# Kernel tuning notes

Measured on AMD Instinct MI355X. Metric: run time of the kernel, lower is better.

## Reference

```python
import jax, jax.numpy as jnp
import numpy as np

N = 40000   # nodes
E = 150000  # edges (before self-loops)
G = 128     # graphs in batch
V = 20000   # vocab
D = 512     # embedding/hidden dim
H = 4       # heads (layers 0,1)
C = 128     # per-head channels (H*C = D)


def setup_inputs() -> dict:
    key = jax.random.key(0)
    ks = jax.random.split(key, 64)
    n = lambda i, shp, s=0.05: jax.random.normal(ks[i], shp, dtype=jnp.float32) * s
    inp = {}
    inp['node_ids'] = jax.random.randint(ks[0], (N,), 0, V, dtype=jnp.int32)
    inp['edge_index'] = jax.random.randint(ks[1], (2, E), 0, N, dtype=jnp.int32)
    inp['batch'] = jnp.sort(jax.random.randint(ks[2], (N,), 0, G, dtype=jnp.int32))
    inp['emb'] = n(3, (V, D), 0.02)
    # GAT layer 0: D -> H x C, concat
    inp['W0'] = n(4, (D, H * C)); inp['as0'] = n(5, (H, C)); inp['ad0'] = n(6, (H, C)); inp['b0'] = n(7, (D,), 0.01)
    # GAT layer 1: D -> H x C, concat
    inp['W1'] = n(8, (D, H * C)); inp['as1'] = n(9, (H, C)); inp['ad1'] = n(10, (H, C)); inp['b1'] = n(11, (D,), 0.01)
    inp['W2'] = n(12, (D, D)); inp['as2'] = n(13, (1, D)); inp['ad2'] = n(14, (1, D)); inp['b2'] = n(15, (D,), 0.01)
    # danger head
    inp['dW1'] = n(16, (D, D)); inp['db1'] = n(17, (D,), 0.01)
    inp['dg1'] = 1.0 + n(18, (D,), 0.02); inp['dbt1'] = n(19, (D,), 0.02)
    inp['drm1'] = n(20, (D,), 0.02); inp['drv1'] = jax.random.uniform(ks[21], (D,)) + 0.5
    inp['dW2'] = n(22, (D, D // 2)); inp['db2'] = n(23, (D // 2,), 0.01)
    inp['dg2'] = 1.0 + n(24, (D // 2,), 0.02); inp['dbt2'] = n(25, (D // 2,), 0.02)
    inp['drm2'] = n(26, (D // 2,), 0.02); inp['drv2'] = jax.random.uniform(ks[27], (D // 2,)) + 0.5
    inp['dW3'] = n(28, (D // 2, 1)); inp['db3'] = n(29, (1,), 0.01)
    # synergy head
    inp['sW1'] = n(30, (D, D)); inp['sb1'] = n(31, (D,), 0.01)
    inp['sg1'] = 1.0 + n(32, (D,), 0.02); inp['sbt1'] = n(33, (D,), 0.02)
    inp['srm1'] = n(34, (D,), 0.02); inp['srv1'] = jax.random.uniform(ks[35], (D,)) + 0.5
    inp['sW2'] = n(36, (D, D // 2)); inp['sb2'] = n(37, (D // 2,), 0.01)
    inp['sg2'] = 1.0 + n(38, (D // 2,), 0.02); inp['sbt2'] = n(39, (D // 2,), 0.02)
    inp['srm2'] = n(40, (D // 2,), 0.02); inp['srv2'] = jax.random.uniform(ks[41], (D // 2,)) + 0.5
    inp['sW3'] = n(42, (D // 2, 1)); inp['sb3'] = n(43, (1,), 0.01)
    return inp


def _gat(x, W, a_src, a_dst, bias, src, dst, heads, ch, concat):
    # PyG GATConv (eval): linear, per-head additive attention, softmax over
    # incoming edges per destination node, scatter-add aggregate.
    n_nodes = x.shape[0]
    h = (x @ W).reshape(n_nodes, heads, ch)              # [N,H,C]
    e_s = jnp.sum(h * a_src, axis=-1)                    # [N,H]
    e_d = jnp.sum(h * a_dst, axis=-1)                    # [N,H]
    e = jax.nn.leaky_relu(e_s[src] + e_d[dst], 0.2)      # [E,H]
    m = jax.ops.segment_max(e, dst, num_segments=n_nodes)
    m = jnp.where(jnp.isfinite(m), m, 0.0)
    p = jnp.exp(e - m[dst])
    s = jax.ops.segment_sum(p, dst, num_segments=n_nodes)
    alpha = p / (s[dst] + 1e-16)                         # [E,H]
    out = jax.ops.segment_sum(h[src] * alpha[:, :, None], dst, num_segments=n_nodes)
    out = out.reshape(n_nodes, heads * ch) if concat else out.mean(axis=1)
    return out + bias


def _bn(x, g, b, rm, rv):
    return (x - rm) * jax.lax.rsqrt(rv + 1e-5) * g + b


def _head(p, W1, b1, g1, bt1, rm1, rv1, W2, b2, g2, bt2, rm2, rv2, W3, b3):
    z = jax.nn.relu(_bn(p @ W1 + b1, g1, bt1, rm1, rv1))
    z = jax.nn.relu(_bn(z @ W2 + b2, g2, bt2, rm2, rv2))
    return jax.nn.sigmoid(z @ W3 + b3)


def reference(node_ids, edge_index, batch, emb, W0, as0, ad0, b0, W1, as1, ad1, b1, W2, as2, ad2, b2, dW1, db1, dg1, dbt1, drm1, drv1, dW2, db2, dg2, dbt2, drm2, drv2, dW3, db3, sW1, sb1, sg1, sbt1, srm1, srv1, sW2, sb2, sg2, sbt2, srm2, srv2, sW3, sb3):
    loops = jnp.arange(N, dtype=edge_index.dtype)
    src = jnp.concatenate([edge_index[0], loops])
    dst = jnp.concatenate([edge_index[1], loops])
    x = emb[node_ids]                                    # [N,D]
    # layer 0 (no residual)
    x = jax.nn.relu(_gat(x, W0, as0, ad0, b0, src, dst, H, C, True))
    # layer 1 (+residual)
    x = x + jax.nn.relu(_gat(x, W1, as1, ad1, b1, src, dst, H, C, True))
    # layer 2 (+residual)
    x = x + jax.nn.relu(_gat(x, W2, as2, ad2, b2, src, dst, 1, D, False))
    # global mean pool per graph
    sums = jax.ops.segment_sum(x, batch, num_segments=G)
    cnt = jax.ops.segment_sum(jnp.ones((N,), x.dtype), batch, num_segments=G)
    pooled = sums / jnp.maximum(cnt, 1.0)[:, None]       # [G,D]
    danger = _head(pooled, dW1, db1, dg1, dbt1, drm1, drv1, dW2, db2, dg2, dbt2, drm2, drv2, dW3, db3)
    synergy = _head(pooled, sW1, sb1, sg1, sbt1, srm1, srv1, sW2, sb2, sg2, sbt2, srm2, srv2, sW3, sb3)
    return danger, synergy
```

## Files before the change

### kernel.cpp

```cpp
#include <hip/hip_runtime.h>
#include <hip/hip_bf16.h>
#include <stdint.h>

#define NN 40000
#define EE 150000
#define ET 190000
#define GG 128
#define DD 512
#define MP 40064
#define PS 16
#define GNB 1252
#define GNBF 1248
#define WB 192
#define CW 32

typedef __hip_bfloat16 bf16;
typedef __attribute__((ext_vector_type(8))) short s16x8;
typedef __attribute__((ext_vector_type(4))) float f32v4;

__device__ __forceinline__ float b2f(bf16 v) { return __bfloat162float(v); }
__device__ __forceinline__ bf16  f2b(float v) { return __float2bfloat16(v); }
__device__ __forceinline__ unsigned f2bu(float v) {
    bf16 b = __float2bfloat16(v);
    return (unsigned)*(unsigned short*)&b;
}
__device__ __forceinline__ float lo16(unsigned u) { return __uint_as_float(u << 16); }
__device__ __forceinline__ float hi16(unsigned u) { return __uint_as_float(u & 0xffff0000u); }
__device__ __forceinline__ float s2f(short s) {
    return __uint_as_float(((unsigned)(unsigned short)s) << 16);
}

__device__ __forceinline__ void gl_lds16(const void* g, void* l) {
    __builtin_amdgcn_global_load_lds(
        (const __attribute__((address_space(1))) unsigned int*)g,
        (__attribute__((address_space(3))) unsigned int*)l, 16, 0, 0);
}

__global__ __launch_bounds__(256) void k_prep(const float* __restrict__ W0,
                                              const float* __restrict__ W1,
                                              const float* __restrict__ W2,
                                              bf16* __restrict__ Wt0,
                                              bf16* __restrict__ Wt1,
                                              bf16* __restrict__ Wt2,
                                              const int* __restrict__ ids,
                                              const float4* __restrict__ emb4,
                                              bf16* __restrict__ xb) {
    __shared__ float tile[64][65];
    int b = blockIdx.x, tid = threadIdx.x;
    if (b < WB) {
        int wi = b >> 6, tl = b & 63;
        const float* W; bf16* Wt;
        if (wi == 0)      { W = W0; Wt = Wt0; }
        else if (wi == 1) { W = W1; Wt = Wt1; }
        else              { W = W2; Wt = Wt2; }
        int n0 = (tl & 7) * 64, k0 = (tl >> 3) * 64;
        int rr = tid >> 4, cc = (tid & 15) * 4;
        #pragma unroll
        for (int i = 0; i < 4; i++) {
            int k = k0 + i * 16 + rr;
            float4 v = *(const float4*)(W + (size_t)k * DD + n0 + cc);
            tile[cc + 0][i * 16 + rr] = v.x;
            tile[cc + 1][i * 16 + rr] = v.y;
            tile[cc + 2][i * 16 + rr] = v.z;
            tile[cc + 3][i * 16 + rr] = v.w;
        }
        __syncthreads();
        #pragma unroll
        for (int i = 0; i < 4; i++) {
            int nl = i * 16 + rr;
            ushort4 o;
            o.x = (unsigned short)f2bu(tile[nl][cc + 0]);
            o.y = (unsigned short)f2bu(tile[nl][cc + 1]);
            o.z = (unsigned short)f2bu(tile[nl][cc + 2]);
            o.w = (unsigned short)f2bu(tile[nl][cc + 3]);
            *(ushort4*)(Wt + (size_t)(n0 + nl) * DD + k0 + cc) = o;
        }
    } else {
        int t = (b - WB) * 256 + tid;
        int n = t >> 7, c = t & 127;
        if (n >= NN) return;
        int id = ids[n];
        float4 v = emb4[(size_t)id * 128 + c];
        ushort4 u;
        u.x = (unsigned short)f2bu(v.x); u.y = (unsigned short)f2bu(v.y);
        u.z = (unsigned short)f2bu(v.z); u.w = (unsigned short)f2bu(v.w);
        *(ushort4*)(xb + (size_t)n * DD + c * 4) = u;
    }
}

__global__ __launch_bounds__(256) void k_fill_fixed(const int* __restrict__ esrc,
                                                    const int* __restrict__ edst,
                                                    int* __restrict__ deg,
                                                    int* __restrict__ csrf) {
    int e = blockIdx.x * 256 + threadIdx.x;
    if (e >= ET) return;
    int dst, src;
    if (e < EE) { dst = edst[e]; src = esrc[e]; }
    else        { dst = e - EE;  src = dst; }
    int slot = atomicAdd(&deg[dst], 1);
    if (slot < CW) csrf[dst * CW + slot] = src;
}

template <int H>
__global__ __launch_bounds__(256) void k_gemm_mfma(const bf16* __restrict__ A,
                                                   const bf16* __restrict__ Bt,
                                                   bf16* __restrict__ C,
                                                   const float* __restrict__ a_s,
                                                   const float* __restrict__ a_d,
                                                   float* __restrict__ es,
                                                   float* __restrict__ ed) {
    constexpr int K = DD, N = DD;
    __shared__ bf16 smem[4 * 128 * 64];
    bf16* lA0 = smem;
    bf16* lB0 = smem + 8192;
    bf16* lA1 = smem + 16384;
    bf16* lB1 = smem + 24576;
    int tid = threadIdx.x, lane = tid & 63, quad = lane >> 4, l16 = lane & 15;
    int w = tid >> 6;

    int bid = blockIdx.x, mt, nt;
    if (bid >= GNBF) { mt = MP / 128 - 1; nt = bid - GNBF; }
    else { nt = (bid & 31) >> 3; mt = (bid >> 5) * 8 + (bid & 7); }
    int m0 = mt * 128, n0 = nt * 128;
    int wm = (w & 1) * 64, wn = (w >> 1) * 64;

    int l8 = lane >> 3, c16 = (lane & 7) << 4;
    int scol = c16 ^ (l8 << 4);
    const char* pAg = (const char*)A + (size_t)(m0 + w * 32 + l8) * (K * 2) + scol;
    const char* pBg = (const char*)Bt + (size_t)(n0 + w * 32 + l8) * (K * 2) + scol;
    char* dA0 = (char*)lA0 + w * 4096;
    char* dB0 = (char*)lB0 + w * 4096;
    char* dA1 = (char*)lA1 + w * 4096;
    char* dB1 = (char*)lB1 + w * 4096;

    int aoff[2][4], boff[2][4];
    #pragma unroll
    for (int kk = 0; kk < 2; kk++)
        #pragma unroll
        for (int i = 0; i < 4; i++) {
            int qb = (kk * 4 + quad) << 4;
            int rowA = wm + i * 16 + l16;
            int rowB = wn + i * 16 + l16;
            aoff[kk][i] = rowA * 64 + ((qb ^ ((rowA & 7) << 4)) >> 1);
            boff[kk][i] = rowB * 64 + ((qb ^ ((rowB & 7) << 4)) >> 1);
        }

    f32v4 zero = 0;
    f32v4 acc[4][4];
    #pragma unroll
    for (int i = 0; i < 4; i++)
        #pragma unroll
        for (int j = 0; j < 4; j++) acc[i][j] = zero;

    auto stage = [&](int kb, char* dA, char* dB) {
        #pragma unroll
        for (int i = 0; i < 4; i++) {
            gl_lds16(pAg + i * 8192 + kb, dA + i * 1024);
            gl_lds16(pBg + i * 8192 + kb, dB + i * 1024);
        }
    };
    auto compute = [&](const bf16* bA, const bf16* bB) {
        #pragma unroll
        for (int kk = 0; kk < 2; kk++) {
            s16x8 a[4], b[4];
            #pragma unroll
            for (int i = 0; i < 4; i++) a[i] = *(const s16x8*)(bA + aoff[kk][i]);
            #pragma unroll
            for (int j = 0; j < 4; j++) b[j] = *(const s16x8*)(bB + boff[kk][j]);
            #pragma unroll
            for (int i = 0; i < 4; i++)
                #pragma unroll
                for (int j = 0; j < 4; j++)
                    acc[i][j] = __builtin_amdgcn_mfma_f32_16x16x32_bf16(a[i], b[j], acc[i][j], 0, 0, 0);
        }
    };

    stage(0, dA0, dB0);
    __syncthreads();
    #pragma unroll
    for (int k0 = 0; k0 < K; k0 += 128) {
        stage((k0 + 64) * 2, dA1, dB1);
        compute(lA0, lB0);
        __syncthreads();
        if (k0 + 128 < K) stage((k0 + 128) * 2, dA0, dB0);
        compute(lA1, lB1);
        __syncthreads();
    }

    float* asl = (float*)(smem + 8192);
    float* adl = asl + 128;
    if (tid < 128) asl[tid] = a_s[n0 + tid];
    else           adl[tid - 128] = a_d[n0 + tid - 128];

    constexpr int ESTR = 136;
    bf16* ebuf = smem;
    int lrB = (w & 1) * 16 + quad * 4;
    int lr = tid >> 3, cc8 = (tid & 7) * 16;
    int grow = m0 + (lr >> 4) * 64 + (lr & 15);
    #pragma unroll
    for (int i = 0; i < 4; i++) {
        __syncthreads();
        #pragma unroll
        for (int j = 0; j < 4; j++) {
            int col = wn + j * 16 + l16;
            #pragma unroll
            for (int r = 0; r < 4; r++)
                ebuf[(lrB + r) * ESTR + col] = f2b(acc[i][j][r]);
        }
        __syncthreads();
        s16x8 v0 = *(s16x8*)(ebuf + lr * ESTR + cc8);
        s16x8 v1 = *(s16x8*)(ebuf + lr * ESTR + cc8 + 8);
        float ses = 0.f, sed = 0.f;
        #pragma unroll
        for (int k = 0; k < 8; k++) {
            float x = s2f(v0[k]);
            ses += x * asl[cc8 + k];
            sed += x * adl[cc8 + k];
        }
        #pragma unroll
        for (int k = 0; k < 8; k++) {
            float x = s2f(v1[k]);
            ses += x * asl[cc8 + 8 + k];
            sed += x * adl[cc8 + 8 + k];
        }
        #pragma unroll
        for (int off = 1; off < 8; off <<= 1) {
            ses += __shfl_xor(ses, off, 64);
            sed += __shfl_xor(sed, off, 64);
        }
        int row = grow + i * 16;
        if ((tid & 7) == 0) {
            if (H == 4) {
                es[(size_t)row * 4 + nt] = ses;
                ed[(size_t)row * 4 + nt] = sed;
            } else {
                es[(size_t)nt * MP + row] = ses;
                ed[(size_t)nt * MP + row] = sed;
            }
        }
        size_t o = (size_t)row * N + n0 + cc8;
        *(s16x8*)(C + o) = v0;
        *(s16x8*)(C + o + 8) = v1;
    }
}

template <int H, bool RES>
__global__ __launch_bounds__(256) void k_gat_aggregate(const bf16* __restrict__ h,
                                                       const float* __restrict__ es,
                                                       const float* __restrict__ ed,
                                                       const int* __restrict__ degv,
                                                       const int* __restrict__ csrf,
                                                       const float* __restrict__ bias,
                                                       bf16* __restrict__ xb) {
    __shared__ int   s_src[8][32];
    __shared__ float s_a[8][32 * H];
    __shared__ int   s_deg[8];
    int tid = threadIdx.x, w = tid >> 6, lane = tid & 63;
    int half = lane >> 5, el = lane & 31;
    int nb = blockIdx.x * 8;
    {
        int ln = w * 2 + half;
        int node = nb + ln;
        int deg = degv[node];
        if (deg > CW) deg = CW;
        if (el == 0) s_deg[ln] = deg;
        float edl[H];
        if (H == 4) {
            #pragma unroll
            for (int hh = 0; hh < H; hh++) edl[hh] = ed[node * H + hh];
        } else {
            edl[0] = ed[node] + ed[MP + node] + ed[2 * MP + node] + ed[3 * MP + node];
        }
        float e_h[H];
        #pragma unroll
        for (int hh = 0; hh < H; hh++) e_h[hh] = -1e30f;
        if (el < deg) {
            int src = csrf[node * CW + el];
            s_src[ln][el] = src;
            if (H == 4) {
                float4 e4 = *(const float4*)(es + (size_t)src * 4);
                float t4[4] = {e4.x, e4.y, e4.z, e4.w};
                #pragma unroll
                for (int hh = 0; hh < 4; hh++) {
                    float e = t4[hh] + edl[hh];
                    e_h[hh] = e > 0.f ? e : 0.2f * e;
                }
            } else {
                float esv = es[src] + es[MP + src] + es[2 * MP + src] + es[3 * MP + src];
                float e = esv + edl[0];
                e_h[0] = e > 0.f ? e : 0.2f * e;
            }
        }
        float m[H];
        #pragma unroll
        for (int hh = 0; hh < H; hh++) m[hh] = e_h[hh];
        #pragma unroll
        for (int off = 16; off; off >>= 1)
            #pragma unroll
            for (int hh = 0; hh < H; hh++) m[hh] = fmaxf(m[hh], __shfl_xor(m[hh], off, 64));
        float p[H], sum[H];
        #pragma unroll
        for (int hh = 0; hh < H; hh++) {
            p[hh] = (el < deg) ? __expf(e_h[hh] - m[hh]) : 0.f;
            sum[hh] = p[hh];
        }
        #pragma unroll
        for (int off = 16; off; off >>= 1)
            #pragma unroll
            for (int hh = 0; hh < H; hh++) sum[hh] += __shfl_xor(sum[hh], off, 64);
        if (el < deg)
            #pragma unroll
            for (int hh = 0; hh < H; hh++) s_a[ln][el * H + hh] = p[hh] / (sum[hh] + 1e-16f);
    }
    __syncthreads();

    int dbase = lane * 8;
    int hd = (H == 4) ? (lane >> 4) : 0;
    float4 bi0 = *(const float4*)(bias + dbase);
    float4 bi1 = *(const float4*)(bias + dbase + 4);
    int ln0 = w * 2, ln1 = w * 2 + 1;
    int deg0 = s_deg[ln0], deg1 = s_deg[ln1];
    int dmax = deg0 > deg1 ? deg0 : deg1;
    float A0[8] = {}, A1[8] = {};
    for (int i = 0; i < dmax; i++) {
        if (i < deg0) {
            uint4 u = *(const uint4*)(h + (size_t)s_src[ln0][i] * DD + dbase);
            float a = s_a[ln0][i * H + hd];
            A0[0] += a * lo16(u.x); A0[1] += a * hi16(u.x);
            A0[2] += a * lo16(u.y); A0[3] += a * hi16(u.y);
            A0[4] += a * lo16(u.z); A0[5] += a * hi16(u.z);
            A0[6] += a * lo16(u.w); A0[7] += a * hi16(u.w);
        }
        if (i < deg1) {
            uint4 u = *(const uint4*)(h + (size_t)s_src[ln1][i] * DD + dbase);
            float a = s_a[ln1][i * H + hd];
            A1[0] += a * lo16(u.x); A1[1] += a * hi16(u.x);
            A1[2] += a * lo16(u.y); A1[3] += a * hi16(u.y);
            A1[4] += a * lo16(u.z); A1[5] += a * hi16(u.z);
            A1[6] += a * lo16(u.w); A1[7] += a * hi16(u.w);
        }
    }
    #pragma unroll
    for (int t = 0; t < 2; t++) {
        float* A = (t == 0) ? A0 : A1;
        int nn = w * 2 + t;
        float v[8];
        v[0] = A[0] + bi0.x; v[1] = A[1] + bi0.y;
        v[2] = A[2] + bi0.z; v[3] = A[3] + bi0.w;
        v[4] = A[4] + bi1.x; v[5] = A[5] + bi1.y;
        v[6] = A[6] + bi1.z; v[7] = A[7] + bi1.w;
        #pragma unroll
        for (int k = 0; k < 8; k++) v[k] = fmaxf(v[k], 0.f);
        size_t base = (size_t)(nb + nn) * DD + dbase;
        if (RES) {
            uint4 u = *(const uint4*)(xb + base);
            v[0] += lo16(u.x); v[1] += hi16(u.x);
            v[2] += lo16(u.y); v[3] += hi16(u.y);
            v[4] += lo16(u.z); v[5] += hi16(u.z);
            v[6] += lo16(u.w); v[7] += hi16(u.w);
        }
        uint4 o;
        o.x = f2bu(v[0]) | (f2bu(v[1]) << 16);
        o.y = f2bu(v[2]) | (f2bu(v[3]) << 16);
        o.z = f2bu(v[4]) | (f2bu(v[5]) << 16);
        o.w = f2bu(v[6]) | (f2bu(v[7]) << 16);
        *(uint4*)(xb + base) = o;
    }
}

__global__ __launch_bounds__(256) void k_pool_part(const int* __restrict__ batch,
                                                   const bf16* __restrict__ xb,
                                                   float* __restrict__ psum,
                                                   int* __restrict__ cnt) {
    int g = blockIdx.x, s = blockIdx.y;
    __shared__ int s_lo, s_hi;
    if (threadIdx.x == 0) {
        int lo = 0, hi = NN;
        while (lo < hi) { int mid = (lo + hi) >> 1; if (batch[mid] < g) lo = mid + 1; else hi = mid; }
        s_lo = lo;
        lo = 0; hi = NN;
        while (lo < hi) { int mid = (lo + hi) >> 1; if (batch[mid] < g + 1) lo = mid + 1; else hi = mid; }
        s_hi = lo;
    }
    __syncthreads();
    int lo = s_lo, hi = s_hi, len = hi - lo;
    int na = lo + (int)(((long)len * s) / PS);
    int nb = lo + (int)(((long)len * (s + 1)) / PS);
    int d0 = threadIdx.x * 2;
    float a0 = 0.f, a1 = 0.f;
    for (int n = na; n < nb; n++) {
        unsigned u = *(const unsigned*)(xb + (size_t)n * DD + d0);
        a0 += lo16(u);
        a1 += hi16(u);
    }
    size_t o = ((size_t)s * GG + g) * DD + d0;
    psum[o]     = a0;
    psum[o + 1] = a1;
    if (s == 0 && threadIdx.x == 0) cnt[g] = len;
}

template <int Din, int Dout, bool FIRST>
__global__ __launch_bounds__(256) void k_head_layer2(const float* __restrict__ inD,
                                                     const float* __restrict__ inS,
                                                     const int* __restrict__ cnt,
                                                     const float* __restrict__ Wd, const float* __restrict__ bd,
                                                     const float* __restrict__ gd, const float* __restrict__ btd,
                                                     const float* __restrict__ rmd, const float* __restrict__ rvd,
                                                     const float* __restrict__ Ws, const float* __restrict__ bs_,
                                                     const float* __restrict__ gs, const float* __restrict__ bts,
                                                     const float* __restrict__ rms, const float* __restrict__ rvs,
                                                     float* __restrict__ outD,
                                                     float* __restrict__ outS) {
    const float *in, *W, *b, *ga, *bt, *rm, *rv; float* out;
    if (blockIdx.z == 0) { in = inD; W = Wd; b = bd; ga = gd; bt = btd; rm = rmd; rv = rvd; out = outD; }
    else                 { in = inS; W = Ws; b = bs_; ga = gs; bt = bts; rm = rms; rv = rvs; out = outS; }
    int g = blockIdx.y;
    int tid = threadIdx.x;
    int j = blockIdx.x * 64 + (tid & 63);
    int ks = tid >> 6;
    __shared__ float s_in[Din];
    __shared__ float s_red[256];
    if (FIRST) {
        float inv = 1.f / fmaxf((float)cnt[g], 1.f);
        for (int k = tid; k < Din; k += 256) {
            float s = 0.f;
            #pragma unroll
            for (int seg = 0; seg < PS; seg++)
                s += in[(size_t)seg * GG * DD + (size_t)g * DD + k];
            s_in[k] = s * inv;
        }
    } else {
        for (int k = tid; k < Din; k += 256) s_in[k] = in[(size_t)g * Din + k];
    }
    __syncthreads();
    constexpr int KS = Din / 4;
    const float* Wp = W + (size_t)ks * KS * Dout + j;
    float acc = 0.f;
    #pragma unroll 8
    for (int k = 0; k < KS; k++) acc += s_in[ks * KS + k] * Wp[(size_t)k * Dout];
    s_red[tid] = acc;
    __syncthreads();
    if (tid < 64) {
        float s = s_red[tid] + s_red[tid + 64] + s_red[tid + 128] + s_red[tid + 192];
        s += b[j];
        s = (s - rm[j]) * rsqrtf(rv[j] + 1e-5f) * ga[j] + bt[j];
        out[(size_t)g * Dout + j] = s > 0.f ? s : 0.f;
    }
}

__global__ __launch_bounds__(64) void k_head_final2(const float* __restrict__ zD,
                                                    const float* __restrict__ zS,
                                                    const float* __restrict__ W3d, const float* __restrict__ b3d,
                                                    const float* __restrict__ W3s, const float* __restrict__ b3s,
                                                    float* __restrict__ out, int Din) {
    const float* z; const float* W3; const float* b3; float* o;
    if (blockIdx.y == 0) { z = zD; W3 = W3d; b3 = b3d; o = out; }
    else                 { z = zS; W3 = W3s; b3 = b3s; o = out + GG; }
    int g = blockIdx.x, lane = threadIdx.x;
    float s = 0.f;
    for (int k = lane; k < Din; k += 64) s += z[(size_t)g * Din + k] * W3[k];
    #pragma unroll
    for (int off = 32; off; off >>= 1) s += __shfl_xor(s, off, 64);
    if (lane == 0) {
        s += b3[0];
        o[g] = 1.f / (1.f + __expf(-s));
    }
}

extern "C" void kernel_launch(void* const* d_in, const int* in_sizes, int n_in,
                              void* d_out, int out_size, void* d_ws, size_t ws_size,
                              hipStream_t stream) {
    const int*   node_ids = (const int*)d_in[0];
    const int*   ei       = (const int*)d_in[1];
    const int*   batch    = (const int*)d_in[2];
    const float* emb      = (const float*)d_in[3];
    const float* W0  = (const float*)d_in[4],  *as0 = (const float*)d_in[5];
    const float* ad0 = (const float*)d_in[6],  *b0  = (const float*)d_in[7];
    const float* W1  = (const float*)d_in[8],  *as1 = (const float*)d_in[9];
    const float* ad1 = (const float*)d_in[10], *b1  = (const float*)d_in[11];
    const float* W2  = (const float*)d_in[12], *as2 = (const float*)d_in[13];
    const float* ad2 = (const float*)d_in[14], *b2  = (const float*)d_in[15];
    const float* dW1 = (const float*)d_in[16], *db1 = (const float*)d_in[17];
    const float* dg1 = (const float*)d_in[18], *dbt1= (const float*)d_in[19];
    const float* drm1= (const float*)d_in[20], *drv1= (const float*)d_in[21];
    const float* dW2 = (const float*)d_in[22], *db2 = (const float*)d_in[23];
    const float* dg2 = (const float*)d_in[24], *dbt2= (const float*)d_in[25];
    const float* drm2= (const float*)d_in[26], *drv2= (const float*)d_in[27];
    const float* dW3 = (const float*)d_in[28], *db3 = (const float*)d_in[29];
    const float* sW1 = (const float*)d_in[30], *sb1 = (const float*)d_in[31];
    const float* sg1 = (const float*)d_in[32], *sbt1= (const float*)d_in[33];
    const float* srm1= (const float*)d_in[34], *srv1= (const float*)d_in[35];
    const float* sW2 = (const float*)d_in[36], *sb2 = (const float*)d_in[37];
    const float* sg2 = (const float*)d_in[38], *sbt2= (const float*)d_in[39];
    const float* srm2= (const float*)d_in[40], *srv2= (const float*)d_in[41];
    const float* sW3 = (const float*)d_in[42], *sb3 = (const float*)d_in[43];

    const int* esrc = ei;
    const int* edst = ei + EE;

    char* p = (char*)d_ws;
    auto alloc = [&](size_t bytes) { char* r = p; p += (bytes + 255) & ~(size_t)255; return (void*)r; };
    bf16*  xb      = (bf16*)alloc((size_t)MP * DD * 2);
    bf16*  hbuf    = (bf16*)alloc((size_t)MP * DD * 2);
    bf16*  Wt0     = (bf16*)alloc((size_t)DD * DD * 2);
    bf16*  Wt1     = (bf16*)alloc((size_t)DD * DD * 2);
    bf16*  Wt2     = (bf16*)alloc((size_t)DD * DD * 2);
    float* esed    = (float*)alloc((size_t)6 * MP * 4 * 4);
    float* es0 = esed,              *ed0 = esed + (size_t)MP * 4;
    float* es1 = esed + (size_t)MP * 8,  *ed1 = esed + (size_t)MP * 12;
    float* es2 = esed + (size_t)MP * 16, *ed2 = esed + (size_t)MP * 20;
    int*   deg     = (int*)alloc((size_t)NN * 4);
    int*   csrf    = (int*)alloc((size_t)NN * CW * 4);
    float* psum    = (float*)alloc((size_t)PS * GG * DD * 4);
    int*   cnt     = (int*)alloc((size_t)GG * 4);
    float* z1d     = (float*)alloc((size_t)GG * DD * 4);
    float* z1s     = (float*)alloc((size_t)GG * DD * 4);
    float* z2d     = (float*)alloc((size_t)GG * 256 * 4);
    float* z2s     = (float*)alloc((size_t)GG * 256 * 4);

    hipMemsetAsync(deg, 0, (size_t)NN * 4, stream);
    k_fill_fixed<<<(ET + 255) / 256, 256, 0, stream>>>(esrc, edst, deg, csrf);

    k_prep<<<WB + (NN * 128 + 255) / 256, 256, 0, stream>>>(W0, W1, W2, Wt0, Wt1, Wt2,
                                                            node_ids, (const float4*)emb, xb);

    k_gemm_mfma<4><<<GNB, 256, 0, stream>>>(xb, Wt0, hbuf, as0, ad0, es0, ed0);
    k_gat_aggregate<4, false><<<NN / 8, 256, 0, stream>>>(hbuf, es0, ed0, deg, csrf, b0, xb);

    k_gemm_mfma<4><<<GNB, 256, 0, stream>>>(xb, Wt1, hbuf, as1, ad1, es1, ed1);
    k_gat_aggregate<4, true><<<NN / 8, 256, 0, stream>>>(hbuf, es1, ed1, deg, csrf, b1, xb);

    k_gemm_mfma<1><<<GNB, 256, 0, stream>>>(xb, Wt2, hbuf, as2, ad2, es2, ed2);
    k_gat_aggregate<1, true><<<NN / 8, 256, 0, stream>>>(hbuf, es2, ed2, deg, csrf, b2, xb);

    dim3 ppgrid(GG, PS);
    k_pool_part<<<ppgrid, 256, 0, stream>>>(batch, xb, psum, cnt);

    float* outp = (float*)d_out;
    dim3 h1grid(DD / 64, GG, 2);
    k_head_layer2<DD, DD, true><<<h1grid, 256, 0, stream>>>(psum, psum, cnt,
        dW1, db1, dg1, dbt1, drm1, drv1,
        sW1, sb1, sg1, sbt1, srm1, srv1, z1d, z1s);
    dim3 h2grid(256 / 64, GG, 2);
    k_head_layer2<DD, 256, false><<<h2grid, 256, 0, stream>>>(z1d, z1s, cnt,
        dW2, db2, dg2, dbt2, drm2, drv2,
        sW2, sb2, sg2, sbt2, srm2, srv2, z2d, z2s);
    dim3 fgrid(GG, 2);
    k_head_final2<<<fgrid, 64, 0, stream>>>(z2d, z2s, dW3, db3, sW3, sb3, outp, 256);
}
```

Baseline: 451.4 us.

## Widen GEMM block tile to 128x256 with eight waves sharing A

The projection GEMM now uses 512-thread blocks that each compute a 128x256 output tile instead of 128x128, halving the number of blocks. Each A row-tile is loaded once and reused across two head-column tiles, which cuts redundant global and LDS staging of activations. The epilogue is reworked so the attention-score dot products still come out per 128-column head chunk. The LDS footprint grows to about 96KB per block, which may limit residency, and the grid gets coarser, which can worsen tail balance across CUs.

```diff
diff --git a/kernel.cpp b/kernel.cpp
--- a/kernel.cpp
+++ b/kernel.cpp
@@ -9,8 +9,7 @@
 #define DD 512
 #define MP 40064
 #define PS 16
-#define GNB 1252
-#define GNBF 1248
+#define GNB2 626
 #define WB 192
 #define CW 32
 
@@ -102,7 +101,7 @@
 }
 
 template <int H>
-__global__ __launch_bounds__(256) void k_gemm_mfma(const bf16* __restrict__ A,
+__global__ __launch_bounds__(512) void k_gemm_mfma(const bf16* __restrict__ A,
                                                    const bf16* __restrict__ Bt,
                                                    bf16* __restrict__ C,
                                                    const float* __restrict__ a_s,
@@ -110,27 +109,26 @@
                                                    float* __restrict__ es,
                                                    float* __restrict__ ed) {
     constexpr int K = DD, N = DD;
-    __shared__ bf16 smem[4 * 128 * 64];
+    __shared__ bf16 smem[49152];
     bf16* lA0 = smem;
     bf16* lB0 = smem + 8192;
-    bf16* lA1 = smem + 16384;
-    bf16* lB1 = smem + 24576;
+    bf16* lA1 = smem + 24576;
+    bf16* lB1 = smem + 32768;
     int tid = threadIdx.x, lane = tid & 63, quad = lane >> 4, l16 = lane & 15;
     int w = tid >> 6;
 
-    int bid = blockIdx.x, mt, nt;
-    if (bid >= GNBF) { mt = MP / 128 - 1; nt = bid - GNBF; }
-    else { nt = (bid & 31) >> 3; mt = (bid >> 5) * 8 + (bid & 7); }
-    int m0 = mt * 128, n0 = nt * 128;
+    int bid = blockIdx.x;
+    int mt = bid >> 1, ntp = bid & 1;
+    int m0 = mt * 128, n0p = ntp * 256;
     int wm = (w & 1) * 64, wn = (w >> 1) * 64;
 
     int l8 = lane >> 3, c16 = (lane & 7) << 4;
     int scol = c16 ^ (l8 << 4);
-    const char* pAg = (const char*)A + (size_t)(m0 + w * 32 + l8) * (K * 2) + scol;
-    const char* pBg = (const char*)Bt + (size_t)(n0 + w * 32 + l8) * (K * 2) + scol;
-    char* dA0 = (char*)lA0 + w * 4096;
+    const char* pAg = (const char*)A + (size_t)(m0 + w * 16 + l8) * (K * 2) + scol;
+    const char* pBg = (const char*)Bt + (size_t)(n0p + w * 32 + l8) * (K * 2) + scol;
+    char* dA0 = (char*)lA0 + w * 2048;
     char* dB0 = (char*)lB0 + w * 4096;
-    char* dA1 = (char*)lA1 + w * 4096;
+    char* dA1 = (char*)lA1 + w * 2048;
     char* dB1 = (char*)lB1 + w * 4096;
 
     int aoff[2][4], boff[2][4];
@@ -154,10 +152,11 @@
 
     auto stage = [&](int kb, char* dA, char* dB) {
         #pragma unroll
-        for (int i = 0; i < 4; i++) {
+        for (int i = 0; i < 2; i++)
             gl_lds16(pAg + i * 8192 + kb, dA + i * 1024);
+        #pragma unroll
+        for (int i = 0; i < 4; i++)
             gl_lds16(pBg + i * 8192 + kb, dB + i * 1024);
-        }
     };
     auto compute = [&](const bf16* bA, const bf16* bB) {
         #pragma unroll
@@ -187,16 +186,17 @@
         __syncthreads();
     }
 
-    float* asl = (float*)(smem + 8192);
-    float* adl = asl + 128;
-    if (tid < 128) asl[tid] = a_s[n0 + tid];
-    else           adl[tid - 128] = a_d[n0 + tid - 128];
-
-    constexpr int ESTR = 136;
+    float* asl = (float*)(smem + 16384);
+    float* adl = asl + 256;
+    if (tid < 256) asl[tid] = a_s[n0p + tid];
+    else           adl[tid - 256] = a_d[n0p + tid - 256];
+
+    constexpr int ESTR = 264;
     bf16* ebuf = smem;
     int lrB = (w & 1) * 16 + quad * 4;
-    int lr = tid >> 3, cc8 = (tid & 7) * 16;
+    int lr = tid >> 4, cc8 = (tid & 15) * 16;
     int grow = m0 + (lr >> 4) * 64 + (lr & 15);
+    int hn = ntp * 2 + ((tid >> 3) & 1);
     #pragma unroll
     for (int i = 0; i < 4; i++) {
         __syncthreads();
@@ -231,14 +231,14 @@
         int row = grow + i * 16;
         if ((tid & 7) == 0) {
             if (H == 4) {
-                es[(size_t)row * 4 + nt] = ses;
-                ed[(size_t)row * 4 + nt] = sed;
+                es[(size_t)row * 4 + hn] = ses;
+                ed[(size_t)row * 4 + hn] = sed;
             } else {
-                es[(size_t)nt * MP + row] = ses;
-                ed[(size_t)nt * MP + row] = sed;
+                es[(size_t)hn * MP + row] = ses;
+                ed[(size_t)hn * MP + row] = sed;
             }
         }
-        size_t o = (size_t)row * N + n0 + cc8;
+        size_t o = (size_t)row * N + n0p + cc8;
         *(s16x8*)(C + o) = v0;
         *(s16x8*)(C + o + 8) = v1;
     }
@@ -524,13 +524,13 @@
     k_prep<<<WB + (NN * 128 + 255) / 256, 256, 0, stream>>>(W0, W1, W2, Wt0, Wt1, Wt2,
                                                             node_ids, (const float4*)emb, xb);
 
-    k_gemm_mfma<4><<<GNB, 256, 0, stream>>>(xb, Wt0, hbuf, as0, ad0, es0, ed0);
+    k_gemm_mfma<4><<<GNB2, 512, 0, stream>>>(xb, Wt0, hbuf, as0, ad0, es0, ed0);
     k_gat_aggregate<4, false><<<NN / 8, 256, 0, stream>>>(hbuf, es0, ed0, deg, csrf, b0, xb);
 
-    k_gemm_mfma<4><<<GNB, 256, 0, stream>>>(xb, Wt1, hbuf, as1, ad1, es1, ed1);
+    k_gemm_mfma<4><<<GNB2, 512, 0, stream>>>(xb, Wt1, hbuf, as1, ad1, es1, ed1);
     k_gat_aggregate<4, true><<<NN / 8, 256, 0, stream>>>(hbuf, es1, ed1, deg, csrf, b1, xb);
 
-    k_gemm_mfma<1><<<GNB, 256, 0, stream>>>(xb, Wt2, hbuf, as2, ad2, es2, ed2);
+    k_gemm_mfma<1><<<GNB2, 512, 0, stream>>>(xb, Wt2, hbuf, as2, ad2, es2, ed2);
     k_gat_aggregate<1, true><<<NN / 8, 256, 0, stream>>>(hbuf, es2, ed2, deg, csrf, b2, xb);
 
     dim3 ppgrid(GG, PS);
```

Result: slower. 477.0 us (+5.7%).

## Fuse global mean pooling into final GAT aggregate via shared-memory and atomic partial sums

Applied to the files above, without the earlier changes.

The last GAT aggregation no longer writes the final node features to xb. It accumulates each block's 8 nodes into per-graph sums, reducing in shared memory when a node belongs to the block's first graph and using global atomics otherwise, then adds to a zeroed psum. This removes the separate pooling kernel along with the write and re-read of the full node-feature tensor. The first head layer now computes graph node counts with a binary search instead of reading them from a buffer. The cost is many float atomics into a small psum array, and summation order becomes nondeterministic.

```diff
diff --git a/kernel.cpp b/kernel.cpp
--- a/kernel.cpp
+++ b/kernel.cpp
@@ -8,7 +8,6 @@
 #define GG 128
 #define DD 512
 #define MP 40064
-#define PS 16
 #define GNB 1252
 #define GNBF 1248
 #define WB 192
@@ -244,26 +243,35 @@
     }
 }
 
-template <int H, bool RES>
+template <int H, bool RES, bool FUSE>
 __global__ __launch_bounds__(256) void k_gat_aggregate(const bf16* __restrict__ h,
                                                        const float* __restrict__ es,
                                                        const float* __restrict__ ed,
                                                        const int* __restrict__ degv,
                                                        const int* __restrict__ csrf,
                                                        const float* __restrict__ bias,
-                                                       bf16* __restrict__ xb) {
+                                                       bf16* __restrict__ xb,
+                                                       const int* __restrict__ batch,
+                                                       float* __restrict__ psum) {
     __shared__ int   s_src[8][32];
     __shared__ float s_a[8][32 * H];
     __shared__ int   s_deg[8];
+    __shared__ int   s_gb[FUSE ? 8 : 1];
+    __shared__ int   s_g0;
+    __shared__ float s_acc[FUSE ? 4 : 1][FUSE ? 8 : 1][FUSE ? 64 : 1];
     int tid = threadIdx.x, w = tid >> 6, lane = tid & 63;
     int half = lane >> 5, el = lane & 31;
     int nb = blockIdx.x * 8;
+    if (FUSE && tid == 0) s_g0 = batch[nb];
     {
         int ln = w * 2 + half;
         int node = nb + ln;
         int deg = degv[node];
         if (deg > CW) deg = CW;
-        if (el == 0) s_deg[ln] = deg;
+        if (el == 0) {
+            s_deg[ln] = deg;
+            if (FUSE) s_gb[ln] = batch[node];
+        }
         float edl[H];
         if (H == 4) {
             #pragma unroll
@@ -321,6 +329,10 @@
     int ln0 = w * 2, ln1 = w * 2 + 1;
     int deg0 = s_deg[ln0], deg1 = s_deg[ln1];
     int dmax = deg0 > deg1 ? deg0 : deg1;
+    if (FUSE) {
+        #pragma unroll
+        for (int k = 0; k < 8; k++) s_acc[w][k][lane] = 0.f;
+    }
     float A0[8] = {}, A1[8] = {};
     for (int i = 0; i < dmax; i++) {
         if (i < deg0) {
@@ -359,50 +371,42 @@
             v[4] += lo16(u.z); v[5] += hi16(u.z);
             v[6] += lo16(u.w); v[7] += hi16(u.w);
         }
-        uint4 o;
-        o.x = f2bu(v[0]) | (f2bu(v[1]) << 16);
-        o.y = f2bu(v[2]) | (f2bu(v[3]) << 16);
-        o.z = f2bu(v[4]) | (f2bu(v[5]) << 16);
-        o.w = f2bu(v[6]) | (f2bu(v[7]) << 16);
-        *(uint4*)(xb + base) = o;
-    }
-}
-
-__global__ __launch_bounds__(256) void k_pool_part(const int* __restrict__ batch,
-                                                   const bf16* __restrict__ xb,
-                                                   float* __restrict__ psum,
-                                                   int* __restrict__ cnt) {
-    int g = blockIdx.x, s = blockIdx.y;
-    __shared__ int s_lo, s_hi;
-    if (threadIdx.x == 0) {
-        int lo = 0, hi = NN;
-        while (lo < hi) { int mid = (lo + hi) >> 1; if (batch[mid] < g) lo = mid + 1; else hi = mid; }
-        s_lo = lo;
-        lo = 0; hi = NN;
-        while (lo < hi) { int mid = (lo + hi) >> 1; if (batch[mid] < g + 1) lo = mid + 1; else hi = mid; }
-        s_hi = lo;
-    }
-    __syncthreads();
-    int lo = s_lo, hi = s_hi, len = hi - lo;
-    int na = lo + (int)(((long)len * s) / PS);
-    int nb = lo + (int)(((long)len * (s + 1)) / PS);
-    int d0 = threadIdx.x * 2;
-    float a0 = 0.f, a1 = 0.f;
-    for (int n = na; n < nb; n++) {
-        unsigned u = *(const unsigned*)(xb + (size_t)n * DD + d0);
-        a0 += lo16(u);
-        a1 += hi16(u);
-    }
-    size_t o = ((size_t)s * GG + g) * DD + d0;
-    psum[o]     = a0;
-    psum[o + 1] = a1;
-    if (s == 0 && threadIdx.x == 0) cnt[g] = len;
+        if (FUSE) {
+            int gn = s_gb[nn];
+            if (gn == s_g0) {
+                #pragma unroll
+                for (int k = 0; k < 8; k++) s_acc[w][k][lane] += v[k];
+            } else {
+                #pragma unroll
+                for (int k = 0; k < 8; k++)
+                    atomicAdd(&psum[(size_t)gn * DD + dbase + k], v[k]);
+            }
+        } else {
+            uint4 o;
+            o.x = f2bu(v[0]) | (f2bu(v[1]) << 16);
+            o.y = f2bu(v[2]) | (f2bu(v[3]) << 16);
+            o.z = f2bu(v[4]) | (f2bu(v[5]) << 16);
+            o.w = f2bu(v[6]) | (f2bu(v[7]) << 16);
+            *(uint4*)(xb + base) = o;
+        }
+    }
+    if (FUSE) {
+        __syncthreads();
+        int d = tid << 1;
+        float a0 = s_acc[0][d & 7][d >> 3] + s_acc[1][d & 7][d >> 3]
+                 + s_acc[2][d & 7][d >> 3] + s_acc[3][d & 7][d >> 3];
+        int d1 = d + 1;
+        float a1 = s_acc[0][d1 & 7][d1 >> 3] + s_acc[1][d1 & 7][d1 >> 3]
+                 + s_acc[2][d1 & 7][d1 >> 3] + s_acc[3][d1 & 7][d1 >> 3];
+        atomicAdd(&psum[(size_t)s_g0 * DD + d], a0);
+        atomicAdd(&psum[(size_t)s_g0 * DD + d1], a1);
+    }
 }
 
 template <int Din, int Dout, bool FIRST>
 __global__ __launch_bounds__(256) void k_head_layer2(const float* __restrict__ inD,
                                                      const float* __restrict__ inS,
-                                                     const int* __restrict__ cnt,
+                                                     const int* __restrict__ batch,
                                                      const float* __restrict__ Wd, const float* __restrict__ bd,
                                                      const float* __restrict__ gd, const float* __restrict__ btd,
                                                      const float* __restrict__ rmd, const float* __restrict__ rvd,
@@ -420,15 +424,17 @@
     int ks = tid >> 6;
     __shared__ float s_in[Din];
     __shared__ float s_red[256];
+    __shared__ float s_inv;
     if (FIRST) {
-        float inv = 1.f / fmaxf((float)cnt[g], 1.f);
-        for (int k = tid; k < Din; k += 256) {
-            float s = 0.f;
-            #pragma unroll
-            for (int seg = 0; seg < PS; seg++)
-                s += in[(size_t)seg * GG * DD + (size_t)g * DD + k];
-            s_in[k] = s * inv;
-        }
+        if (tid == 0) {
+            int lo = 0, hi = NN;
+            while (lo < hi) { int mid = (lo + hi) >> 1; if (batch[mid] < g) lo = mid + 1; else hi = mid; }
+            int a = lo; lo = 0; hi = NN;
+            while (lo < hi) { int mid = (lo + hi) >> 1; if (batch[mid] < g + 1) lo = mid + 1; else hi = mid; }
+            s_inv = 1.f / fmaxf((float)(lo - a), 1.f);
+        }
+        __syncthreads();
+        for (int k = tid; k < Din; k += 256) s_in[k] = in[(size_t)g * DD + k] * s_inv;
     } else {
         for (int k = tid; k < Din; k += 256) s_in[k] = in[(size_t)g * Din + k];
     }
@@ -511,38 +517,35 @@
     float* es2 = esed + (size_t)MP * 16, *ed2 = esed + (size_t)MP * 20;
     int*   deg     = (int*)alloc((size_t)NN * 4);
     int*   csrf    = (int*)alloc((size_t)NN * CW * 4);
-    float* psum    = (float*)alloc((size_t)PS * GG * DD * 4);
-    int*   cnt     = (int*)alloc((size_t)GG * 4);
+    float* psum    = (float*)alloc((size_t)GG * DD * 4);
     float* z1d     = (float*)alloc((size_t)GG * DD * 4);
     float* z1s     = (float*)alloc((size_t)GG * DD * 4);
     float* z2d     = (float*)alloc((size_t)GG * 256 * 4);
     float* z2s     = (float*)alloc((size_t)GG * 256 * 4);
 
     hipMemsetAsync(deg, 0, (size_t)NN * 4, stream);
+    hipMemsetAsync(psum, 0, (size_t)GG * DD * 4, stream);
     k_fill_fixed<<<(ET + 255) / 256, 256, 0, stream>>>(esrc, edst, deg, csrf);
 
     k_prep<<<WB + (NN * 128 + 255) / 256, 256, 0, stream>>>(W0, W1, W2, Wt0, Wt1, Wt2,
                                                             node_ids, (const float4*)emb, xb);
 
     k_gemm_mfma<4><<<GNB, 256, 0, stream>>>(xb, Wt0, hbuf, as0, ad0, es0, ed0);
-    k_gat_aggregate<4, false><<<NN / 8, 256, 0, stream>>>(hbuf, es0, ed0, deg, csrf, b0, xb);
+    k_gat_aggregate<4, false, false><<<NN / 8, 256, 0, stream>>>(hbuf, es0, ed0, deg, csrf, b0, xb, nullptr, nullptr);
 
     k_gemm_mfma<4><<<GNB, 256, 0, stream>>>(xb, Wt1, hbuf, as1, ad1, es1, ed1);
-    k_gat_aggregate<4, true><<<NN / 8, 256, 0, stream>>>(hbuf, es1, ed1, deg, csrf, b1, xb);
+    k_gat_aggregate<4, true, false><<<NN / 8, 256, 0, stream>>>(hbuf, es1, ed1, deg, csrf, b1, xb, nullptr, nullptr);
 
     k_gemm_mfma<1><<<GNB, 256, 0, stream>>>(xb, Wt2, hbuf, as2, ad2, es2, ed2);
-    k_gat_aggregate<1, true><<<NN / 8, 256, 0, stream>>>(hbuf, es2, ed2, deg, csrf, b2, xb);
-
-    dim3 ppgrid(GG, PS);
-    k_pool_part<<<ppgrid, 256, 0, stream>>>(batch, xb, psum, cnt);
+    k_gat_aggregate<1, true, true><<<NN / 8, 256, 0, stream>>>(hbuf, es2, ed2, deg, csrf, b2, xb, batch, psum);
 
     float* outp = (float*)d_out;
     dim3 h1grid(DD / 64, GG, 2);
-    k_head_layer2<DD, DD, true><<<h1grid, 256, 0, stream>>>(psum, psum, cnt,
+    k_head_layer2<DD, DD, true><<<h1grid, 256, 0, stream>>>(psum, psum, batch,
         dW1, db1, dg1, dbt1, drm1, drv1,
         sW1, sb1, sg1, sbt1, srm1, srv1, z1d, z1s);
     dim3 h2grid(256 / 64, GG, 2);
-    k_head_layer2<DD, 256, false><<<h2grid, 256, 0, stream>>>(z1d, z1s, cnt,
+    k_head_layer2<DD, 256, false><<<h2grid, 256, 0, stream>>>(z1d, z1s, batch,
         dW2, db2, dg2, dbt2, drm2, drv2,
         sW2, sb2, sg2, sbt2, srm2, srv2, z2d, z2s);
     dim3 fgrid(GG, 2);
```

Measured after the change: 450.2 us. About the same (-0.3%).
